# Kernel optimization log

Hardware: AMD Instinct MI355X
Metric: run time of the kernel (lower is better)

## Reference

```python
import jax, jax.numpy as jnp
import numpy as np

B, LATENT, HID, OUT, E = 8192, 128, 400, 4096, 16

def setup_inputs() -> dict:
    key = jax.random.key(0)
    k = jax.random.split(key, 6)
    return {
        "z": jax.random.normal(k[0], (B, LATENT), dtype=jnp.float32),
        "W1": jax.random.normal(k[1], (E, HID, LATENT), dtype=jnp.float32) * (1.0 / np.sqrt(LATENT)),
        "b1": jax.random.normal(k[2], (E, HID), dtype=jnp.float32) * 0.01,
        "W2": jax.random.normal(k[3], (E, OUT, HID), dtype=jnp.float32) * (1.0 / np.sqrt(HID)),
        "b2": jax.random.normal(k[4], (E, OUT), dtype=jnp.float32) * 0.01,
        "angle_idx": jax.random.randint(k[5], (B,), 0, E, dtype=jnp.int64) if jax.config.jax_enable_x64 else jax.random.randint(k[5], (B,), 0, E, dtype=jnp.int32),
    }

def reference(z, W1, b1, W2, b2, angle_idx):
    # Per-sample expert select: out[i] = sigmoid(W2[e] @ relu(W1[e] @ z[i] + b1[e]) + b2[e]), e = angle_idx[i].
    # Dense-dispatch reference: run every expert on the full batch, select per-sample result.
    n_experts = W1.shape[0]
    out = jnp.zeros((z.shape[0], W2.shape[1]), dtype=z.dtype)
    for e in range(n_experts):  # small fixed loop over experts
        h = jax.nn.relu(z @ W1[e].T + b1[e])          # [B, 400]
        o = jax.nn.sigmoid(h @ W2[e].T + b2[e])       # [B, OUT]
        out = jnp.where((angle_idx == e)[:, None], o, out)
    return out
```

## Files before the change

kernel.cpp:

```cpp
#include <hip/hip_runtime.h>

#define BATCH  8192
#define LATENT 128
#define HID    400
#define HIDB   400
#define HIDP   448
#define NOUT   4096
#define NE     16
#define HROWS  (BATCH + 256)

typedef __attribute__((ext_vector_type(8))) short bf16x8;
typedef __attribute__((ext_vector_type(4))) float f32x4;

__device__ __forceinline__ unsigned short f2bf(float f){
  unsigned u = __builtin_bit_cast(unsigned, f);
  u += 0x7fffu + ((u >> 16) & 1u);
  return (unsigned short)(u >> 16);
}

__device__ __forceinline__ void gload16(const void* g, void* l){
  __builtin_amdgcn_global_load_lds(
      (const __attribute__((address_space(1))) void*)g,
      (__attribute__((address_space(3))) void*)l, 16, 0, 0);
}

__global__ __launch_bounds__(1024) void k_prep(
    const int* __restrict__ aidx, int* __restrict__ wsI,
    const float* __restrict__ W2, unsigned short* __restrict__ W2b)
{
  int tid = threadIdx.x;
  if (blockIdx.x != 0){
    const int NCH = NE*NOUT*HIDB/8;
    int g = ((int)blockIdx.x - 1)*1024 + tid;
    for (int i = g; i < NCH; i += 1536*1024){
      const float* s = W2 + (size_t)i*8;
      f32x4 a = __builtin_nontemporal_load((const f32x4*)s);
      f32x4 b = __builtin_nontemporal_load((const f32x4*)(s+4));
      bf16x8 w;
      w[0]=(short)f2bf(a.x); w[1]=(short)f2bf(a.y); w[2]=(short)f2bf(a.z); w[3]=(short)f2bf(a.w);
      w[4]=(short)f2bf(b.x); w[5]=(short)f2bf(b.y); w[6]=(short)f2bf(b.z); w[7]=(short)f2bf(b.w);
      __builtin_nontemporal_store(w, (bf16x8*)(W2b + (size_t)i*8));
    }
    return;
  }
  __shared__ int hist[NE];
  __shared__ int cursor[NE];
  int lane = tid & 63;
  if (tid < NE) hist[tid] = 0;
  __syncthreads();

  int ev[8];
  #pragma unroll
  for (int c=0;c<8;c++) ev[c] = aidx[c*1024 + tid];

  #pragma unroll
  for (int c=0;c<8;c++){
    for (int x=0;x<NE;x++){
      unsigned long long m = __ballot(ev[c]==x);
      if (lane==0 && m) atomicAdd(&hist[x], (int)__popcll(m));
    }
  }
  __syncthreads();
  if (tid==0){
    int a=0;
    for (int x=0;x<NE;x++){ cursor[x]=a; wsI[32+x]=a; a+=hist[x]; }
    wsI[32+NE]=a;
  }
  __syncthreads();

  #pragma unroll
  for (int c=0;c<8;c++){
    int e = ev[c], i = c*1024 + tid;
    for (int x=0;x<NE;x++){
      unsigned long long m = __ballot(e==x);
      if (m){
        int leader = __ffsll((unsigned long long)m) - 1;
        int base = 0;
        if (lane == leader) base = atomicAdd(&cursor[x], (int)__popcll(m));
        base = __shfl(base, leader);
        if (e==x){
          int rank = (int)__popcll(m & ((1ull<<lane)-1ull));
          wsI[64 + base + rank] = i;
        }
      }
    }
  }
}

__global__ __launch_bounds__(256) void k_layer1(
    const float* __restrict__ z, const float* __restrict__ W1, const float* __restrict__ b1,
    const int* __restrict__ wsI, unsigned short* __restrict__ hws)
{
  __shared__ int s_off[NE+1];
  __shared__ int s_perm[64];
  __shared__ unsigned short As[64*128];
  __shared__ unsigned short Bs[64*128];
  int tid = threadIdx.x;
  if (tid <= NE) s_off[tid] = wsI[32+tid];
  __syncthreads();

  int e=-1, tile=0;
  { int acc=0;
    for (int i=0;i<NE;i++){
      int cnt = s_off[i+1]-s_off[i]; int t = (cnt+63)>>6;
      if ((int)blockIdx.x < acc+t){ e=i; tile=(int)blockIdx.x-acc; break; }
      acc += t; } }
  if (e < 0) return;
  int r0 = s_off[e] + tile*64;
  int rows = s_off[e+1] - r0; if (rows > 64) rows = 64;
  int n0 = blockIdx.y * 64;

  if (tid < 64) s_perm[tid] = (tid < rows) ? wsI[64 + r0 + tid] : 0;
  __syncthreads();

  #pragma unroll
  for (int p=0;p<8;p++){
    int id = tid + p*256; int row = id>>5, c4 = id&31;
    float4 v = make_float4(0.f,0.f,0.f,0.f);
    if (row < rows) v = *(const float4*)(z + (size_t)s_perm[row]*LATENT + c4*4);
    short4 w; w.x=(short)f2bf(v.x); w.y=(short)f2bf(v.y); w.z=(short)f2bf(v.z); w.w=(short)f2bf(v.w);
    *(short4*)((char*)As + row*256 + ((c4*8) ^ ((row&7)<<4))) = w;
  }
  const float* w1e = W1 + (size_t)e*HID*LATENT;
  #pragma unroll
  for (int p=0;p<8;p++){
    int id = tid + p*256; int row = id>>5, c4 = id&31;
    int n = n0 + row;
    float4 v = make_float4(0.f,0.f,0.f,0.f);
    if (n < HID) v = *(const float4*)(w1e + (size_t)n*LATENT + c4*4);
    short4 w; w.x=(short)f2bf(v.x); w.y=(short)f2bf(v.y); w.z=(short)f2bf(v.z); w.w=(short)f2bf(v.w);
    *(short4*)((char*)Bs + row*256 + ((c4*8) ^ ((row&7)<<4))) = w;
  }
  __syncthreads();

  int lane = tid & 63, wid = tid >> 6;
  int wm = wid >> 1, wn = wid & 1;
  int llo = lane & 15, lhi = lane >> 4;
  f32x4 acc[2][2];
  #pragma unroll
  for (int i=0;i<2;i++)
    #pragma unroll
    for (int j=0;j<2;j++) acc[i][j] = (f32x4){0.f,0.f,0.f,0.f};

  #pragma unroll
  for (int s=0;s<4;s++){
    bf16x8 af[2], bfr[2];
    #pragma unroll
    for (int i=0;i<2;i++){ int m = wm*32 + i*16 + llo;
      af[i] = *(bf16x8*)((char*)As + m*256 + ((s*64 + lhi*16) ^ ((m&7)<<4))); }
    #pragma unroll
    for (int j=0;j<2;j++){ int n = wn*32 + j*16 + llo;
      bfr[j] = *(bf16x8*)((char*)Bs + n*256 + ((s*64 + lhi*16) ^ ((n&7)<<4))); }
    #pragma unroll
    for (int i=0;i<2;i++)
      #pragma unroll
      for (int j=0;j<2;j++)
        acc[i][j] = __builtin_amdgcn_mfma_f32_16x16x32_bf16(af[i], bfr[j], acc[i][j], 0,0,0);
  }

  const float* b1e = b1 + e*HID;
  #pragma unroll
  for (int i=0;i<2;i++){
    #pragma unroll
    for (int j=0;j<2;j++){
      int n = n0 + wn*32 + j*16 + llo;
      float bias = (n < HID) ? b1e[n] : 0.f;
      #pragma unroll
      for (int q=0;q<4;q++){
        int m = wm*32 + i*16 + lhi*4 + q;
        if (m < rows){
          float v = acc[i][j][q] + bias;
          v = (v > 0.f) ? v : 0.f;
          if (n >= HID) v = 0.f;
          hws[(size_t)(r0+m)*HIDP + n] = f2bf(v);
        }
      }
    }
  }
}

__global__ __launch_bounds__(256) void k_layer2(
    const unsigned short* __restrict__ hws, const unsigned short* __restrict__ W2b,
    const float* __restrict__ b2, const int* __restrict__ wsI, float* __restrict__ out)
{
  __shared__ int s_off[NE+1];
  __shared__ int s_perm[128];
  __shared__ unsigned short As[2][128*64];
  __shared__ unsigned short Bs[2][128*64];
  int tid = threadIdx.x;
  if (tid <= NE) s_off[tid] = wsI[32+tid];
  __syncthreads();

  int lin = (int)blockIdx.x;
  int logical = (lin & 7) * 320 + (lin >> 3);
  int bx = logical % 80, by = logical / 80;

  int e=-1, tile=0;
  { int acc=0;
    for (int i=0;i<NE;i++){
      int cnt = s_off[i+1]-s_off[i]; int t = (cnt+127)>>7;
      if (bx < acc+t){ e=i; tile=bx-acc; break; }
      acc += t; } }
  if (e < 0) return;
  int r0 = s_off[e] + tile*128;
  int rows = s_off[e+1] - r0; if (rows > 128) rows = 128;
  int n0 = by * 128;
  if (tid < 128) s_perm[tid] = (tid < rows) ? wsI[64 + r0 + tid] : 0;

  int lane = tid & 63, w = tid >> 6;
  int srow = lane >> 3;
  int colU = (lane & 7) ^ srow;
  const unsigned short* aSrcBase = hws + (size_t)r0*HIDP + colU*8;
  const unsigned short* bSrcBase = W2b + ((size_t)e*NOUT + n0)*HIDB + colU*8;
  int bAdj = (colU >= 2) ? -48 : 0;

  int wm = w >> 1, wn = w & 1;
  int llo = lane & 15, lhi = lane >> 4;
  f32x4 acc[4][4];
  #pragma unroll
  for (int i=0;i<4;i++)
    #pragma unroll
    for (int j=0;j<4;j++) acc[i][j] = (f32x4){0.f,0.f,0.f,0.f};

  #define STAGE(BUF, K0, ADJ) { _Pragma("unroll") for (int p=0;p<4;p++){ \
      int c = w*4 + p; int row = c*8 + srow; \
      gload16(aSrcBase + (size_t)row*HIDP + (K0), &As[BUF][c*512]); \
      gload16(bSrcBase + (size_t)row*HIDB + (K0) + (ADJ), &Bs[BUF][c*512]); } }

  STAGE(0, 0, 0);

  int cur = 0;
  for (int kt=0; kt<7; kt++){
    if (kt < 6){
      STAGE(cur^1, (kt+1)*64, ((kt+1)==6) ? bAdj : 0);
      asm volatile("s_waitcnt vmcnt(8)" ::: "memory");
    } else {
      asm volatile("s_waitcnt vmcnt(0)" ::: "memory");
    }
    __builtin_amdgcn_s_barrier();
    #pragma unroll
    for (int s=0;s<2;s++){
      bf16x8 af[4], bfr[4];
      #pragma unroll
      for (int i=0;i<4;i++){ int m = wm*64 + i*16 + llo;
        af[i] = *(bf16x8*)((char*)&As[cur][0] + m*128 + ((s*64 + lhi*16) ^ ((m&7)<<4))); }
      #pragma unroll
      for (int j=0;j<4;j++){ int n = wn*64 + j*16 + llo;
        bfr[j] = *(bf16x8*)((char*)&Bs[cur][0] + n*128 + ((s*64 + lhi*16) ^ ((n&7)<<4))); }
      #pragma unroll
      for (int i=0;i<4;i++)
        #pragma unroll
        for (int j=0;j<4;j++)
          acc[i][j] = __builtin_amdgcn_mfma_f32_16x16x32_bf16(af[i], bfr[j], acc[i][j], 0,0,0);
    }
    __builtin_amdgcn_s_barrier();
    cur ^= 1;
  }

  const float* b2e = b2 + (size_t)e*NOUT;
  #pragma unroll
  for (int i=0;i<4;i++){
    int mb = wm*64 + i*16 + lhi*4;
    #pragma unroll
    for (int q=0;q<4;q++){
      int m = mb + q;
      if (m < rows){
        int orow = s_perm[m];
        float* op = out + (size_t)orow*NOUT + n0;
        #pragma unroll
        for (int j=0;j<4;j++){
          int nloc = wn*64 + j*16 + llo;
          float x = acc[i][j][q] + b2e[n0 + nloc];
          __builtin_nontemporal_store(1.f / (1.f + __expf(-x)), op + nloc);
        }
      }
    }
  }
}

extern "C" void kernel_launch(void* const* d_in, const int* in_sizes, int n_in,
                              void* d_out, int out_size, void* d_ws, size_t ws_size,
                              hipStream_t stream){
  const float* z   = (const float*)d_in[0];
  const float* W1  = (const float*)d_in[1];
  const float* b1  = (const float*)d_in[2];
  const float* W2  = (const float*)d_in[3];
  const float* b2  = (const float*)d_in[4];
  const int*  aidx = (const int*)d_in[5];
  float* out = (float*)d_out;
  int* wsI = (int*)d_ws;
  unsigned short* hws = (unsigned short*)((char*)d_ws + 65536);
  unsigned short* W2b = (unsigned short*)((char*)d_ws + 65536 + (size_t)HROWS*HIDP*2);

  k_prep  <<<1537, 1024, 0, stream>>>(aidx, wsI, W2, W2b);
  k_layer1<<<dim3(144, 7), 256, 0, stream>>>(z, W1, b1, wsI, hws);
  k_layer2<<<2560, 256, 0, stream>>>(hws, W2b, b2, wsI, out);
}
```

Measured before the change: 161.6 us.

## Pad bf16 W2 to 448 columns and drop layer-2 LDS double buffering

The W2 fp32-to-bf16 conversion now writes a zero-padded 448-wide row layout, so the last K tile needs no per-lane address adjustment. The layer-2 GEMM switches from a double-buffered async LDS pipeline to a single buffer with load, sync, compute, sync per K step. This halves LDS use, which may raise occupancy, and simplifies addressing. In exchange it gives up overlap of global loads with MFMA work and writes a larger padded W2 copy.

```diff
diff --git a/kernel.cpp b/kernel.cpp
--- a/kernel.cpp
+++ b/kernel.cpp
@@ -3,7 +3,6 @@
 #define BATCH  8192
 #define LATENT 128
 #define HID    400
-#define HIDB   400
 #define HIDP   448
 #define NOUT   4096
 #define NE     16
@@ -30,16 +29,21 @@
 {
   int tid = threadIdx.x;
   if (blockIdx.x != 0){
-    const int NCH = NE*NOUT*HIDB/8;
+    const int NSLOT = NE*NOUT*(HIDP/8);
     int g = ((int)blockIdx.x - 1)*1024 + tid;
-    for (int i = g; i < NCH; i += 1536*1024){
-      const float* s = W2 + (size_t)i*8;
-      f32x4 a = __builtin_nontemporal_load((const f32x4*)s);
-      f32x4 b = __builtin_nontemporal_load((const f32x4*)(s+4));
-      bf16x8 w;
-      w[0]=(short)f2bf(a.x); w[1]=(short)f2bf(a.y); w[2]=(short)f2bf(a.z); w[3]=(short)f2bf(a.w);
-      w[4]=(short)f2bf(b.x); w[5]=(short)f2bf(b.y); w[6]=(short)f2bf(b.z); w[7]=(short)f2bf(b.w);
-      __builtin_nontemporal_store(w, (bf16x8*)(W2b + (size_t)i*8));
+    for (int i = g; i < NSLOT; i += 1536*1024){
+      int row  = (int)((unsigned)i / 56u);
+      int slot = i - row*56;
+      int k = slot*8;
+      bf16x8 w = (bf16x8){0,0,0,0,0,0,0,0};
+      if (slot < 50){
+        const float* s = W2 + (size_t)row*HID + k;
+        f32x4 a = __builtin_nontemporal_load((const f32x4*)s);
+        f32x4 b = __builtin_nontemporal_load((const f32x4*)(s+4));
+        w[0]=(short)f2bf(a.x); w[1]=(short)f2bf(a.y); w[2]=(short)f2bf(a.z); w[3]=(short)f2bf(a.w);
+        w[4]=(short)f2bf(b.x); w[5]=(short)f2bf(b.y); w[6]=(short)f2bf(b.z); w[7]=(short)f2bf(b.w);
+      }
+      __builtin_nontemporal_store(w, (bf16x8*)(W2b + (size_t)row*HIDP + k));
     }
     return;
   }
@@ -185,8 +189,8 @@
 {
   __shared__ int s_off[NE+1];
   __shared__ int s_perm[128];
-  __shared__ unsigned short As[2][128*64];
-  __shared__ unsigned short Bs[2][128*64];
+  __shared__ unsigned short As[128*64];
+  __shared__ unsigned short Bs[128*64];
   int tid = threadIdx.x;
   if (tid <= NE) s_off[tid] = wsI[32+tid];
   __syncthreads();
@@ -211,8 +215,7 @@
   int srow = lane >> 3;
   int colU = (lane & 7) ^ srow;
   const unsigned short* aSrcBase = hws + (size_t)r0*HIDP + colU*8;
-  const unsigned short* bSrcBase = W2b + ((size_t)e*NOUT + n0)*HIDB + colU*8;
-  int bAdj = (colU >= 2) ? -48 : 0;
+  const unsigned short* bSrcBase = W2b + ((size_t)e*NOUT + n0)*HIDP + colU*8;
 
   int wm = w >> 1, wn = w & 1;
   int llo = lane & 15, lhi = lane >> 4;
@@ -222,39 +225,30 @@
     #pragma unroll
     for (int j=0;j<4;j++) acc[i][j] = (f32x4){0.f,0.f,0.f,0.f};
 
-  #define STAGE(BUF, K0, ADJ) { _Pragma("unroll") for (int p=0;p<4;p++){ \
+  #define STAGE(K0) { _Pragma("unroll") for (int p=0;p<4;p++){ \
       int c = w*4 + p; int row = c*8 + srow; \
-      gload16(aSrcBase + (size_t)row*HIDP + (K0), &As[BUF][c*512]); \
-      gload16(bSrcBase + (size_t)row*HIDB + (K0) + (ADJ), &Bs[BUF][c*512]); } }
-
-  STAGE(0, 0, 0);
-
-  int cur = 0;
+      gload16(aSrcBase + (size_t)row*HIDP + (K0), &As[c*512]); \
+      gload16(bSrcBase + (size_t)row*HIDP + (K0), &Bs[c*512]); } }
+
   for (int kt=0; kt<7; kt++){
-    if (kt < 6){
-      STAGE(cur^1, (kt+1)*64, ((kt+1)==6) ? bAdj : 0);
-      asm volatile("s_waitcnt vmcnt(8)" ::: "memory");
-    } else {
-      asm volatile("s_waitcnt vmcnt(0)" ::: "memory");
-    }
-    __builtin_amdgcn_s_barrier();
+    STAGE(kt*64);
+    __syncthreads();
     #pragma unroll
     for (int s=0;s<2;s++){
       bf16x8 af[4], bfr[4];
       #pragma unroll
       for (int i=0;i<4;i++){ int m = wm*64 + i*16 + llo;
-        af[i] = *(bf16x8*)((char*)&As[cur][0] + m*128 + ((s*64 + lhi*16) ^ ((m&7)<<4))); }
+        af[i] = *(bf16x8*)((char*)As + m*128 + ((s*64 + lhi*16) ^ ((m&7)<<4))); }
       #pragma unroll
       for (int j=0;j<4;j++){ int n = wn*64 + j*16 + llo;
-        bfr[j] = *(bf16x8*)((char*)&Bs[cur][0] + n*128 + ((s*64 + lhi*16) ^ ((n&7)<<4))); }
+        bfr[j] = *(bf16x8*)((char*)Bs + n*128 + ((s*64 + lhi*16) ^ ((n&7)<<4))); }
       #pragma unroll
       for (int i=0;i<4;i++)
         #pragma unroll
         for (int j=0;j<4;j++)
           acc[i][j] = __builtin_amdgcn_mfma_f32_16x16x32_bf16(af[i], bfr[j], acc[i][j], 0,0,0);
     }
-    __builtin_amdgcn_s_barrier();
-    cur ^= 1;
+    __syncthreads();
   }
 
   const float* b2e = b2 + (size_t)e*NOUT;
```

After: 160.4 us. No clear change (-0.8%).
